# Kernel optimization log

Hardware: AMD Instinct MI355X
Metric: run time of the kernel (lower is better)

## Reference

```python
import jax, jax.numpy as jnp
import numpy as np

NUM_K_HEADS = 16
NUM_V_HEADS = 32
HEAD_K = 64
HEAD_V = 64
KERNEL = 4
KEY_DIM = NUM_K_HEADS * HEAD_K      # 1024
VAL_DIM = NUM_V_HEADS * HEAD_V      # 2048
CONV_DIM = 2 * KEY_DIM + VAL_DIM    # 4096
T = 2048


def setup_inputs() -> dict:
    key = jax.random.key(0)
    ks = jax.random.split(key, 6)
    return {
        "mixed_qkv": jax.random.normal(ks[0], (T, CONV_DIM), jnp.float32),
        "conv_state_in": jnp.zeros((1, KERNEL - 1, CONV_DIM), jnp.float32),
        "recurrent_state_in": jnp.zeros((1, NUM_V_HEADS, HEAD_K, HEAD_V), jnp.float32),
        "b": jax.random.normal(ks[1], (T, NUM_V_HEADS), jnp.float32),
        "a": jax.random.normal(ks[2], (T, NUM_V_HEADS), jnp.float32),
        "conv1d_weight": jax.random.normal(ks[3], (CONV_DIM, KERNEL), jnp.float32) * 0.1,
        "A_log": jax.random.normal(ks[4], (NUM_V_HEADS,), jnp.float32) * 0.1,
        "dt_bias": jax.random.normal(ks[5], (NUM_V_HEADS,), jnp.float32) * 0.1,
    }


def _causal_conv1d_prefill(x, weight, init_state):
    """Depthwise causal conv1d with silu. x:[T,D], weight:[D,W], init_state:[W-1,D]."""
    W = weight.shape[1]
    t = x.shape[0]
    padded = jnp.concatenate([init_state, x], axis=0)  # [T+W-1, D]
    out = padded[0:t] * weight[:, 0]
    for w in range(1, W):  # tiny fixed-width loop (W=4), fused by XLA
        out = out + padded[w:w + t] * weight[:, w]
    return jax.nn.silu(out)


def _l2norm(x, eps=1e-6):
    return x * jax.lax.rsqrt(jnp.sum(x * x, axis=-1, keepdims=True) + eps)


def reference(mixed_qkv, conv_state_in, recurrent_state_in, b, a, conv1d_weight, A_log, dt_bias):
    # --- causal conv over the prefill sequence (batch slice [:1] as in the module) ---
    conv_out = _causal_conv1d_prefill(mixed_qkv, conv1d_weight, conv_state_in[0])  # [T, CONV_DIM]
    t = conv_out.shape[0]

    # --- split into q/k/v heads ---
    q = conv_out[:, :KEY_DIM].reshape(t, NUM_K_HEADS, HEAD_K)
    k = conv_out[:, KEY_DIM:2 * KEY_DIM].reshape(t, NUM_K_HEADS, HEAD_K)
    v = conv_out[:, 2 * KEY_DIM:].reshape(t, NUM_V_HEADS, HEAD_V)
    rep = NUM_V_HEADS // NUM_K_HEADS
    if rep > 1:
        q = jnp.repeat(q, rep, axis=1)
        k = jnp.repeat(k, rep, axis=1)

    # --- gates ---
    beta = jax.nn.sigmoid(b.astype(jnp.float32))                       # [T, H]
    g = -jnp.exp(A_log)[None] * jax.nn.softplus(a.astype(jnp.float32) + dt_bias[None])  # [T, H]

    # --- qk l2-norm and scale (use_qk_l2norm=True) ---
    qn = _l2norm(q) * (HEAD_K ** -0.5)
    kn = _l2norm(k)

    # --- gated delta-rule recurrence over time ---
    def step(S, inp):
        q_t, k_t, v_t, g_t, b_t = inp  # [H,dk],[H,dk],[H,dv],[H],[H]
        S = S * jnp.exp(g_t)[:, None, None]                      # decay
        kv = jnp.einsum('hkv,hk->hv', S, k_t)                    # memory read
        u = b_t[:, None] * (v_t - kv)                            # delta update
        S = S + jnp.einsum('hk,hv->hkv', k_t, u)
        o = jnp.einsum('hkv,hk->hv', S, q_t)
        return S, o

    S0 = recurrent_state_in[0]  # [H, dk, dv]
    _, core_attn_out = jax.lax.scan(step, S0, (qn, kn, v, g, beta))
    return core_attn_out  # [T, H_v, head_v_dim]
```

## Files before the change

kernel.cpp:

```cpp
#include <hip/hip_runtime.h>
#include <math.h>

#define T_LEN   2048
#define NKH     16
#define NVH     32
#define HD      64
#define KEY_DIM 1024
#define VAL_DIM 2048
#define CONV_DIM 4096
#define NCHUNK  32
#define CL      64

typedef float fl4 __attribute__((ext_vector_type(4)));

__device__ __forceinline__ float sigmoid_f(float x) { return 1.f / (1.f + __expf(-x)); }
__device__ __forceinline__ float rdlane(float v, int i) {
    return __int_as_float(__builtin_amdgcn_readlane(__float_as_int(v), i));
}

__global__ __launch_bounds__(256) void prep_kernel(
    const float* __restrict__ x,
    const float* __restrict__ cs,
    const float* __restrict__ w,
    const float* __restrict__ bsrc,
    const float* __restrict__ a,
    const float* __restrict__ A_log,
    const float* __restrict__ dt_bias,
    float* __restrict__ qn,
    float* __restrict__ kn,
    float* __restrict__ vb,
    float* __restrict__ g,
    float* __restrict__ beta)
{
    const int t   = blockIdx.x;
    const int tid = threadIdx.x;
    const int d0  = tid * 16;

    fl4 r4[4];
    #pragma unroll
    for (int grp = 0; grp < 4; ++grp) {
        const int d = d0 + grp * 4;
        fl4 xv[4], wq[4];
        #pragma unroll
        for (int wi = 0; wi < 4; ++wi) {
            const int row = t - 3 + wi;
            const float* src = (row >= 0) ? (x + (size_t)row * CONV_DIM + d)
                                          : (cs + (size_t)(row + 3) * CONV_DIM + d);
            xv[wi] = *(const fl4*)src;
        }
        #pragma unroll
        for (int j = 0; j < 4; ++j) wq[j] = *(const fl4*)(w + (size_t)(d + j) * 4);
        #pragma unroll
        for (int j = 0; j < 4; ++j) {
            float acc = xv[0][j] * wq[j][0];
            acc = fmaf(xv[1][j], wq[j][1], acc);
            acc = fmaf(xv[2][j], wq[j][2], acc);
            acc = fmaf(xv[3][j], wq[j][3], acc);
            r4[grp][j] = acc * sigmoid_f(acc);
        }
    }

    if (tid < 128) {
        float ss = 0.f;
        #pragma unroll
        for (int grp = 0; grp < 4; ++grp)
            #pragma unroll
            for (int j = 0; j < 4; ++j) ss = fmaf(r4[grp][j], r4[grp][j], ss);
        ss += __shfl_xor(ss, 1);
        ss += __shfl_xor(ss, 2);
        const bool is_q = (tid < 64);
        float scale = (is_q ? 0.125f : 1.0f) / sqrtf(ss + 1e-6f);
        float* dst = is_q ? (qn + (size_t)t * KEY_DIM + d0)
                          : (kn + (size_t)t * KEY_DIM + (d0 - KEY_DIM));
        #pragma unroll
        for (int grp = 0; grp < 4; ++grp) {
            fl4 o;
            #pragma unroll
            for (int j = 0; j < 4; ++j) o[j] = r4[grp][j] * scale;
            *(fl4*)(dst + grp * 4) = o;
        }
    } else {
        const int hh = (d0 - 2 * KEY_DIM) >> 6;
        const float bb = sigmoid_f(bsrc[(size_t)t * NVH + hh]);
        float* dst = vb + (size_t)t * VAL_DIM + (d0 - 2 * KEY_DIM);
        #pragma unroll
        for (int grp = 0; grp < 4; ++grp) {
            fl4 o;
            #pragma unroll
            for (int j = 0; j < 4; ++j) o[j] = r4[grp][j] * bb;
            *(fl4*)(dst + grp * 4) = o;
        }
    }

    if (tid < 32) {
        float av = a[(size_t)t * NVH + tid] + dt_bias[tid];
        float sp = fmaxf(av, 0.f) + log1pf(__expf(-fabsf(av)));
        g[(size_t)t * NVH + tid]    = -__expf(A_log[tid]) * sp;
        beta[(size_t)t * NVH + tid] = sigmoid_f(bsrc[(size_t)t * NVH + tid]);
    }
}

__global__ __launch_bounds__(256) void phase1_kernel(
    const float* __restrict__ qn, const float* __restrict__ kn,
    const float* __restrict__ gws, const float* __restrict__ bws,
    float* __restrict__ gam_g, float* __restrict__ bg_g,
    float* __restrict__ KT_g, float* __restrict__ QT_g,
    float* __restrict__ MTt_g, float* __restrict__ SUt_g)
{
    const int bid = blockIdx.x;
    const int c = bid >> 5, h = bid & 31, kh = h >> 1;
    const int tid = threadIdx.x, lane = tid & 63, wv = tid >> 6;

    __shared__ float Ks[64][68], Qs[64][68], Am[64][68], Tm[64][68];
    __shared__ float Gs[64], Dend[64], Bet[64];
    __shared__ float Xs[4][16][17];

    #pragma unroll
    for (int p = 0; p < 4; ++p) {
        int idx = p * 256 + tid;
        int t = idx >> 4, i4 = (idx & 15) * 4;
        *(fl4*)&Ks[t][i4] = *(const fl4*)&kn[(size_t)(c*64+t)*KEY_DIM + kh*64 + i4];
        *(fl4*)&Qs[t][i4] = *(const fl4*)&qn[(size_t)(c*64+t)*KEY_DIM + kh*64 + i4];
    }
    for (int idx = tid; idx < 64*64; idx += 256) {
        int t = idx >> 6, s = idx & 63;
        Tm[t][s] = (t == s) ? 1.f : 0.f;
    }
    if (tid < 64) {
        float gv = gws[(size_t)(c*64+lane)*NVH + h];
        #pragma unroll
        for (int d = 1; d < 64; d <<= 1) {
            float nv = __shfl_up(gv, d);
            if (lane >= d) gv += nv;
        }
        Gs[lane] = gv;
        float g63 = __shfl(gv, 63);
        Dend[lane] = __expf(g63 - gv);
        float bb = bws[(size_t)(c*64+lane)*NVH + h];
        Bet[lane] = bb;
        float ga = __expf(gv);
        gam_g[(size_t)(c*NVH+h)*64 + lane] = ga;
        bg_g[(size_t)(c*NVH+h)*64 + lane]  = ga * bb;
    }
    __syncthreads();

    if ((h & 1) == 0) {
        float* kdst = KT_g + (size_t)(c*NKH + kh)*64*64;
        float* qdst = QT_g + (size_t)(c*NKH + kh)*64*64;
        const int t = lane;
        #pragma unroll
        for (int ii = 0; ii < 16; ++ii) {
            int i = wv*16 + ii;
            kdst[i*64 + t] = Ks[t][i];
            qdst[i*64 + t] = Qs[t][i];
        }
    }

    float accK[16], accQ[16];
    {
        #pragma unroll
        for (int j = 0; j < 16; ++j) { accK[j] = 0.f; accQ[j] = 0.f; }
        const int t = lane, sbase = wv * 16;
        for (int i4 = 0; i4 < 64; i4 += 4) {
            fl4 kt = *(const fl4*)&Ks[t][i4];
            fl4 qt = *(const fl4*)&Qs[t][i4];
            #pragma unroll
            for (int sj = 0; sj < 16; ++sj) {
                fl4 ks = *(const fl4*)&Ks[sbase + sj][i4];
                accK[sj] += kt[0]*ks[0] + kt[1]*ks[1] + kt[2]*ks[2] + kt[3]*ks[3];
                accQ[sj] += qt[0]*ks[0] + qt[1]*ks[1] + qt[2]*ks[2] + qt[3]*ks[3];
            }
        }
    }
    __syncthreads();
    {
        const int t = lane, sbase = wv * 16;
        const float gt = Gs[t], bt = Bet[t];
        #pragma unroll
        for (int sj = 0; sj < 16; ++sj) {
            int s = sbase + sj;
            float e = __expf(gt - Gs[s]);
            Am[t][s] = (s < t)  ? bt * e * accK[sj] : 0.f;
            Qs[t][s] = (s <= t) ? e * accQ[sj] : 0.f;
        }
    }
    __syncthreads();

    {
        const int base = wv * 16;
        const int s = lane & 15;
        float Tc[16];
        #pragma unroll
        for (int j = 0; j < 16; ++j) Tc[j] = (j == s) ? 1.f : 0.f;
        #pragma unroll
        for (int t = 1; t < 16; ++t) {
            float acc = 0.f;
            #pragma unroll
            for (int il = 0; il < 16; ++il) {
                if (il < t) acc = fmaf(Am[base + t][base + il], Tc[il], acc);
            }
            Tc[t] = (s < t) ? -acc : Tc[t];
        }
        if (lane < 16) {
            #pragma unroll
            for (int j = 0; j < 16; ++j)
                Tm[base + j][base + s] = Tc[j];
        }
    }
    for (int L = 1; L <= 3; ++L) {
        __syncthreads();
        if (wv < 4 - L) {
            const int J = wv, I = wv + L;
            const int r = lane & 15, cg = lane >> 4;
            float X[4] = {0.f,0.f,0.f,0.f};
            for (int Kb = J; Kb < I; ++Kb) {
                #pragma unroll
                for (int p = 0; p < 16; ++p) {
                    float av = Am[I*16 + r][Kb*16 + p];
                    #pragma unroll
                    for (int mm = 0; mm < 4; ++mm)
                        X[mm] += av * Tm[Kb*16 + p][J*16 + cg + 4*mm];
                }
            }
            #pragma unroll
            for (int mm = 0; mm < 4; ++mm) Xs[wv][r][cg + 4*mm] = X[mm];
            float Y[4] = {0.f,0.f,0.f,0.f};
            #pragma unroll
            for (int p = 0; p < 16; ++p) {
                float td = Tm[I*16 + r][I*16 + p];
                #pragma unroll
                for (int mm = 0; mm < 4; ++mm)
                    Y[mm] += td * Xs[wv][p][cg + 4*mm];
            }
            #pragma unroll
            for (int mm = 0; mm < 4; ++mm)
                Tm[I*16 + r][J*16 + cg + 4*mm] = -Y[mm];
        }
    }
    __syncthreads();

    {
        float acc[16];
        #pragma unroll
        for (int j = 0; j < 16; ++j) acc[j] = 0.f;
        const int t = lane, sbase = wv * 16;
        for (int i = 0; i < 64; i += 4) {
            fl4 mv4 = *(const fl4*)&Qs[t][i];
            #pragma unroll
            for (int r = 0; r < 4; ++r) {
                fl4 ta = *(const fl4*)&Tm[i+r][sbase + 0];
                fl4 tb = *(const fl4*)&Tm[i+r][sbase + 4];
                fl4 tc = *(const fl4*)&Tm[i+r][sbase + 8];
                fl4 td = *(const fl4*)&Tm[i+r][sbase + 12];
                #pragma unroll
                for (int q = 0; q < 4; ++q) {
                    acc[q]      = fmaf(mv4[r], ta[q], acc[q]);
                    acc[4 + q]  = fmaf(mv4[r], tb[q], acc[4 + q]);
                    acc[8 + q]  = fmaf(mv4[r], tc[q], acc[8 + q]);
                    acc[12 + q] = fmaf(mv4[r], td[q], acc[12 + q]);
                }
            }
        }
        float* dst = MTt_g + (size_t)(c*NVH + h)*64*64;
        #pragma unroll
        for (int sj = 0; sj < 16; ++sj)
            dst[(sbase + sj)*64 + t] = acc[sj];
    }
    {
        float acc[16];
        #pragma unroll
        for (int j = 0; j < 16; ++j) acc[j] = 0.f;
        const int d = lane, sbase = wv * 16;
        for (int t = 0; t < 64; ++t) {
            float kd = Ks[t][d] * Dend[t];
            fl4 ta = *(const fl4*)&Tm[t][sbase + 0];
            fl4 tb = *(const fl4*)&Tm[t][sbase + 4];
            fl4 tc = *(const fl4*)&Tm[t][sbase + 8];
            fl4 td = *(const fl4*)&Tm[t][sbase + 12];
            #pragma unroll
            for (int q = 0; q < 4; ++q) {
                acc[q]      = fmaf(kd, ta[q], acc[q]);
                acc[4 + q]  = fmaf(kd, tb[q], acc[4 + q]);
                acc[8 + q]  = fmaf(kd, tc[q], acc[8 + q]);
                acc[12 + q] = fmaf(kd, td[q], acc[12 + q]);
            }
        }
        float* dst = SUt_g + (size_t)(c*NVH + h)*64*64;
        #pragma unroll
        for (int sj = 0; sj < 16; ++sj)
            dst[(sbase + sj)*64 + d] = acc[sj];
    }
}

__global__ __launch_bounds__(512) void phase2_kernel(
    const float* __restrict__ vbp, const float* __restrict__ gam_g,
    const float* __restrict__ bg_g, const float* __restrict__ KT_g,
    const float* __restrict__ QT_g, const float* __restrict__ MTt_g,
    const float* __restrict__ SUt_g, const float* __restrict__ rs0,
    float* __restrict__ out)
{
    const int bid = blockIdx.x;
    const int h = bid & 31, jg = bid >> 5, kh = h >> 1;
    const int tid = threadIdx.x, lane = tid & 63, wv = tid >> 6;
    const int mv = wv >> 2;
    const int jb = (wv & 3) * 2;

    __shared__ float bufA[8192];
    __shared__ float bufB[8192];
    __shared__ float s0s[64][9], wshs[64][9], o1s[64][9];

    {
        int d = tid >> 3, j = tid & 7;
        s0s[d][j] = rs0[((size_t)h*64 + d)*64 + jg*8 + j];
    }

    const int base = tid * 4;

    fl4 rA0, rA1, rA2, rA3;
    {
        const float* kt = KT_g + (size_t)kh * 4096 + base;
        const float* qt = QT_g + (size_t)kh * 4096 + base;
        rA0 = *(const fl4*)(kt); rA1 = *(const fl4*)(kt + 2048);
        rA2 = *(const fl4*)(qt); rA3 = *(const fl4*)(qt + 2048);
    }

    for (int c = 0; c < NCHUNK; ++c) {
        *(fl4*)&bufA[base       ] = rA0; *(fl4*)&bufA[base + 2048] = rA1;
        *(fl4*)&bufA[base + 4096] = rA2; *(fl4*)&bufA[base + 6144] = rA3;

        fl4 rB0, rB1, rB2, rB3;
        {
            const float* mt = MTt_g + (size_t)(c*NVH + h)*4096 + base;
            const float* su = SUt_g + (size_t)(c*NVH + h)*4096 + base;
            rB0 = *(const fl4*)(mt); rB1 = *(const fl4*)(mt + 2048);
            rB2 = *(const fl4*)(su); rB3 = *(const fl4*)(su + 2048);
        }

        const float* gamc = gam_g + (size_t)(c*NVH + h)*64;
        const float* bgc  = bg_g  + (size_t)(c*NVH + h)*64;
        const float gend = gamc[63];
        float vb0 = 0.f, vb1 = 0.f, bgl = 0.f, gml = 0.f;
        if (mv == 0) {
            const float* vp = &vbp[(size_t)(c*64 + lane)*VAL_DIM + h*64 + jg*8 + jb];
            vb0 = vp[0]; vb1 = vp[1];
            bgl = bgc[lane];
        } else {
            gml = gamc[lane];
        }

        __syncthreads();

        float sa0 = s0s[lane][jb], sa1 = s0s[lane][jb + 1];
        float a0 = 0.f, a1 = 0.f;
        {
            const float* mb = &bufA[mv * 4096 + lane];
            #pragma unroll
            for (int i = 0; i < 64; ++i) {
                float m = mb[i * 64];
                a0 = fmaf(m, rdlane(sa0, i), a0);
                a1 = fmaf(m, rdlane(sa1, i), a1);
            }
        }
        if (mv == 0) {
            wshs[lane][jb]     = vb0 - bgl * a0;
            wshs[lane][jb + 1] = vb1 - bgl * a1;
        } else {
            o1s[lane][jb]     = gml * a0;
            o1s[lane][jb + 1] = gml * a1;
        }
        __syncthreads();

        *(fl4*)&bufB[base       ] = rB0; *(fl4*)&bufB[base + 2048] = rB1;
        *(fl4*)&bufB[base + 4096] = rB2; *(fl4*)&bufB[base + 6144] = rB3;

        if (c + 1 < NCHUNK) {
            const float* kt = KT_g + (size_t)((c+1)*NKH + kh)*4096 + base;
            const float* qt = QT_g + (size_t)((c+1)*NKH + kh)*4096 + base;
            rA0 = *(const fl4*)(kt); rA1 = *(const fl4*)(kt + 2048);
            rA2 = *(const fl4*)(qt); rA3 = *(const fl4*)(qt + 2048);
        }
        __syncthreads();

        float sb0 = wshs[lane][jb], sb1 = wshs[lane][jb + 1];
        float b0 = 0.f, b1 = 0.f;
        {
            const float* mb = &bufB[mv * 4096 + lane];
            #pragma unroll
            for (int i = 0; i < 64; ++i) {
                float m = mb[i * 64];
                b0 = fmaf(m, rdlane(sb0, i), b0);
                b1 = fmaf(m, rdlane(sb1, i), b1);
            }
        }
        if (mv == 0) {
            float* op = &out[(size_t)(c*64 + lane)*VAL_DIM + h*64 + jg*8 + jb];
            op[0] = o1s[lane][jb]     + b0;
            op[1] = o1s[lane][jb + 1] + b1;
        } else {
            s0s[lane][jb]     = gend * s0s[lane][jb]     + b0;
            s0s[lane][jb + 1] = gend * s0s[lane][jb + 1] + b1;
        }
        __syncthreads();
    }
}

#define LOADSTEP(KA, QA, VV, GG, BB, tt) {                                     \
    _Pragma("unroll")                                                          \
    for (int i = 0; i < 4; ++i) {                                              \
        KA[i] = *(const fl4*)(kp + (size_t)(tt) * KEY_DIM + i * 4);            \
        QA[i] = *(const fl4*)(qp + (size_t)(tt) * KEY_DIM + i * 4);            \
    }                                                                          \
    VV = vp[(size_t)(tt) * VAL_DIM];                                           \
    GG = gp[(size_t)(tt) * NVH];                                               \
    BB = bp[(size_t)(tt) * NVH];                                               \
}

#define COMPUTE(KA, QA, VV, GG, BB, tt) {                                      \
    const float dec = __expf(GG);                                              \
    float c0 = 0.f, c1 = 0.f, c2 = 0.f, c3 = 0.f;                              \
    _Pragma("unroll")                                                          \
    for (int i = 0; i < 4; ++i) {                                              \
        S[i*4+0] *= dec; S[i*4+1] *= dec; S[i*4+2] *= dec; S[i*4+3] *= dec;    \
        c0 = fmaf(S[i*4+0], KA[i][0], c0);                                     \
        c1 = fmaf(S[i*4+1], KA[i][1], c1);                                     \
        c2 = fmaf(S[i*4+2], KA[i][2], c2);                                     \
        c3 = fmaf(S[i*4+3], KA[i][3], c3);                                     \
    }                                                                          \
    float kv = (c0 + c1) + (c2 + c3);                                          \
    kv += __shfl_xor(kv, 1);                                                   \
    kv += __shfl_xor(kv, 2);                                                   \
    const float u = VV - BB * kv;                                              \
    float o0 = 0.f, o1 = 0.f, o2 = 0.f, o3 = 0.f;                              \
    _Pragma("unroll")                                                          \
    for (int i = 0; i < 4; ++i) {                                              \
        S[i*4+0] = fmaf(KA[i][0], u, S[i*4+0]);                                \
        S[i*4+1] = fmaf(KA[i][1], u, S[i*4+1]);                                \
        S[i*4+2] = fmaf(KA[i][2], u, S[i*4+2]);                                \
        S[i*4+3] = fmaf(KA[i][3], u, S[i*4+3]);                                \
        o0 = fmaf(S[i*4+0], QA[i][0], o0);                                     \
        o1 = fmaf(S[i*4+1], QA[i][1], o1);                                     \
        o2 = fmaf(S[i*4+2], QA[i][2], o2);                                     \
        o3 = fmaf(S[i*4+3], QA[i][3], o3);                                     \
    }                                                                          \
    float oo = (o0 + o1) + (o2 + o3);                                          \
    oo += __shfl_xor(oo, 1);                                                   \
    oo += __shfl_xor(oo, 2);                                                   \
    if (kg == 0) op[(size_t)(tt) * VAL_DIM] = oo;                              \
}

__global__ __launch_bounds__(256) void scan_kernel(
    const float* __restrict__ qn, const float* __restrict__ kn,
    const float* __restrict__ v, const float* __restrict__ g,
    const float* __restrict__ bet, const float* __restrict__ rs0,
    float* __restrict__ out)
{
    const int h    = blockIdx.x;
    const int kh   = h >> 1;
    const int tid  = threadIdx.x;
    const int vcol = tid >> 2;
    const int kg   = tid & 3;

    float S[16];
    #pragma unroll
    for (int j = 0; j < 16; ++j)
        S[j] = rs0[((size_t)h * HD + (kg * 16 + j)) * HD + vcol];

    const float* kp = kn + (size_t)kh * HD + kg * 16;
    const float* qp = qn + (size_t)kh * HD + kg * 16;
    const float* vp = v + (size_t)h * HD + vcol;
    const float* gp = g + h;
    const float* bp = bet + h;
    float*       op = out + (size_t)h * HD + vcol;

    fl4 ka0[4], qa0[4]; float vv0, gg0, bb0;
    fl4 ka1[4], qa1[4]; float vv1, gg1, bb1;

    LOADSTEP(ka0, qa0, vv0, gg0, bb0, 0);
    for (int t = 0; t < T_LEN; t += 2) {
        LOADSTEP(ka1, qa1, vv1, gg1, bb1, t + 1);
        COMPUTE(ka0, qa0, vv0, gg0, bb0, t);
        const int t2 = (t + 2 < T_LEN) ? (t + 2) : (T_LEN - 1);
        LOADSTEP(ka0, qa0, vv0, gg0, bb0, t2);
        COMPUTE(ka1, qa1, vv1, gg1, bb1, t + 1);
    }
}

extern "C" void kernel_launch(void* const* d_in, const int* in_sizes, int n_in,
                              void* d_out, int out_size, void* d_ws, size_t ws_size,
                              hipStream_t stream)
{
    const float* x       = (const float*)d_in[0];
    const float* cs      = (const float*)d_in[1];
    const float* rs0     = (const float*)d_in[2];
    const float* b       = (const float*)d_in[3];
    const float* a       = (const float*)d_in[4];
    const float* w       = (const float*)d_in[5];
    const float* A_log   = (const float*)d_in[6];
    const float* dt_bias = (const float*)d_in[7];
    float* out = (float*)d_out;

    float* ws = (float*)d_ws;
    size_t off = 0;
    float* qn  = ws + off; off += (size_t)T_LEN * KEY_DIM;
    float* kn  = ws + off; off += (size_t)T_LEN * KEY_DIM;
    float* vb  = ws + off; off += (size_t)T_LEN * VAL_DIM;
    float* g   = ws + off; off += (size_t)T_LEN * NVH;
    float* be  = ws + off; off += (size_t)T_LEN * NVH;
    float* gam = ws + off; off += (size_t)NCHUNK * NVH * 64;
    float* bg  = ws + off; off += (size_t)NCHUNK * NVH * 64;
    float* KT  = ws + off; off += (size_t)NCHUNK * NKH * 64 * 64;
    float* QT  = ws + off; off += (size_t)NCHUNK * NKH * 64 * 64;
    float* MTt = ws + off; off += (size_t)NCHUNK * NVH * 64 * 64;
    float* SUt = ws + off; off += (size_t)NCHUNK * NVH * 64 * 64;
    const size_t need = off * sizeof(float);

    prep_kernel<<<T_LEN, 256, 0, stream>>>(x, cs, w, b, a, A_log, dt_bias,
                                           qn, kn, vb, g, be);
    if (ws_size >= need) {
        phase1_kernel<<<NCHUNK * NVH, 256, 0, stream>>>(qn, kn, g, be,
                                                        gam, bg, KT, QT, MTt, SUt);
        phase2_kernel<<<NVH * 8, 512, 0, stream>>>(vb, gam, bg, KT, QT, MTt, SUt,
                                                   rs0, out);
    } else {
        scan_kernel<<<NVH, 256, 0, stream>>>(qn, kn, vb, g, be, rs0, out);
    }
}
```

Baseline: 283.9 us.

## Share K/Q Gram work across head pairs and prefetch phase2 operands one chunk ahead

phase1 now runs one block per (chunk, key head) and processes both value heads that share that key head. The K/Q loads, the KK^T/QK^T Gram products and the KT/QT transposes are done once and reused for both heads, which halves the block count and removes duplicated work. phase2 prefetches MTt/SUt for the next chunk into registers, removes one __syncthreads per chunk, and splits each dot-product FMA chain into even/odd accumulators to add instruction-level parallelism. In exchange there are fewer blocks in phase1 (less parallelism), more registers live in phase2, and the summation order changes slightly.

```diff
diff --git a/kernel.cpp b/kernel.cpp
--- a/kernel.cpp
+++ b/kernel.cpp
@@ -108,11 +108,11 @@
     float* __restrict__ MTt_g, float* __restrict__ SUt_g)
 {
     const int bid = blockIdx.x;
-    const int c = bid >> 5, h = bid & 31, kh = h >> 1;
+    const int c = bid >> 4, kh = bid & 15;
     const int tid = threadIdx.x, lane = tid & 63, wv = tid >> 6;
 
     __shared__ float Ks[64][68], Qs[64][68], Am[64][68], Tm[64][68];
-    __shared__ float Gs[64], Dend[64], Bet[64];
+    __shared__ float Gs[2][64], Dend[2][64], Bet[2][64];
     __shared__ float Xs[4][16][17];
 
     #pragma unroll
@@ -126,25 +126,27 @@
         int t = idx >> 6, s = idx & 63;
         Tm[t][s] = (t == s) ? 1.f : 0.f;
     }
-    if (tid < 64) {
+    if (tid < 128) {
+        const int hh = wv;
+        const int h = 2*kh + hh;
         float gv = gws[(size_t)(c*64+lane)*NVH + h];
         #pragma unroll
         for (int d = 1; d < 64; d <<= 1) {
             float nv = __shfl_up(gv, d);
             if (lane >= d) gv += nv;
         }
-        Gs[lane] = gv;
+        Gs[hh][lane] = gv;
         float g63 = __shfl(gv, 63);
-        Dend[lane] = __expf(g63 - gv);
+        Dend[hh][lane] = __expf(g63 - gv);
         float bb = bws[(size_t)(c*64+lane)*NVH + h];
-        Bet[lane] = bb;
+        Bet[hh][lane] = bb;
         float ga = __expf(gv);
         gam_g[(size_t)(c*NVH+h)*64 + lane] = ga;
         bg_g[(size_t)(c*NVH+h)*64 + lane]  = ga * bb;
     }
     __syncthreads();
 
-    if ((h & 1) == 0) {
+    {
         float* kdst = KT_g + (size_t)(c*NKH + kh)*64*64;
         float* qdst = QT_g + (size_t)(c*NKH + kh)*64*64;
         const int t = lane;
@@ -172,123 +174,128 @@
             }
         }
     }
-    __syncthreads();
-    {
-        const int t = lane, sbase = wv * 16;
-        const float gt = Gs[t], bt = Bet[t];
-        #pragma unroll
-        for (int sj = 0; sj < 16; ++sj) {
-            int s = sbase + sj;
-            float e = __expf(gt - Gs[s]);
-            Am[t][s] = (s < t)  ? bt * e * accK[sj] : 0.f;
-            Qs[t][s] = (s <= t) ? e * accQ[sj] : 0.f;
-        }
-    }
-    __syncthreads();
-
-    {
-        const int base = wv * 16;
-        const int s = lane & 15;
-        float Tc[16];
-        #pragma unroll
-        for (int j = 0; j < 16; ++j) Tc[j] = (j == s) ? 1.f : 0.f;
-        #pragma unroll
-        for (int t = 1; t < 16; ++t) {
-            float acc = 0.f;
-            #pragma unroll
-            for (int il = 0; il < 16; ++il) {
-                if (il < t) acc = fmaf(Am[base + t][base + il], Tc[il], acc);
-            }
-            Tc[t] = (s < t) ? -acc : Tc[t];
-        }
-        if (lane < 16) {
-            #pragma unroll
-            for (int j = 0; j < 16; ++j)
-                Tm[base + j][base + s] = Tc[j];
-        }
-    }
-    for (int L = 1; L <= 3; ++L) {
+
+    #pragma unroll
+    for (int hh = 0; hh < 2; ++hh) {
+        const int h = 2*kh + hh;
         __syncthreads();
-        if (wv < 4 - L) {
-            const int J = wv, I = wv + L;
-            const int r = lane & 15, cg = lane >> 4;
-            float X[4] = {0.f,0.f,0.f,0.f};
-            for (int Kb = J; Kb < I; ++Kb) {
+        {
+            const int t = lane, sbase = wv * 16;
+            const float gt = Gs[hh][t], bt = Bet[hh][t];
+            #pragma unroll
+            for (int sj = 0; sj < 16; ++sj) {
+                int s = sbase + sj;
+                float e = __expf(gt - Gs[hh][s]);
+                Am[t][s] = (s < t)  ? bt * e * accK[sj] : 0.f;
+                Qs[t][s] = (s <= t) ? e * accQ[sj] : 0.f;
+            }
+        }
+        __syncthreads();
+
+        {
+            const int base = wv * 16;
+            const int s = lane & 15;
+            float Tc[16];
+            #pragma unroll
+            for (int j = 0; j < 16; ++j) Tc[j] = (j == s) ? 1.f : 0.f;
+            #pragma unroll
+            for (int t = 1; t < 16; ++t) {
+                float acc = 0.f;
+                #pragma unroll
+                for (int il = 0; il < 16; ++il) {
+                    if (il < t) acc = fmaf(Am[base + t][base + il], Tc[il], acc);
+                }
+                Tc[t] = (s < t) ? -acc : Tc[t];
+            }
+            if (lane < 16) {
+                #pragma unroll
+                for (int j = 0; j < 16; ++j)
+                    Tm[base + j][base + s] = Tc[j];
+            }
+        }
+        for (int L = 1; L <= 3; ++L) {
+            __syncthreads();
+            if (wv < 4 - L) {
+                const int J = wv, I = wv + L;
+                const int r = lane & 15, cg = lane >> 4;
+                float X[4] = {0.f,0.f,0.f,0.f};
+                for (int Kb = J; Kb < I; ++Kb) {
+                    #pragma unroll
+                    for (int p = 0; p < 16; ++p) {
+                        float av = Am[I*16 + r][Kb*16 + p];
+                        #pragma unroll
+                        for (int mm = 0; mm < 4; ++mm)
+                            X[mm] += av * Tm[Kb*16 + p][J*16 + cg + 4*mm];
+                    }
+                }
+                #pragma unroll
+                for (int mm = 0; mm < 4; ++mm) Xs[wv][r][cg + 4*mm] = X[mm];
+                float Y[4] = {0.f,0.f,0.f,0.f};
                 #pragma unroll
                 for (int p = 0; p < 16; ++p) {
-                    float av = Am[I*16 + r][Kb*16 + p];
+                    float td = Tm[I*16 + r][I*16 + p];
                     #pragma unroll
                     for (int mm = 0; mm < 4; ++mm)
-                        X[mm] += av * Tm[Kb*16 + p][J*16 + cg + 4*mm];
+                        Y[mm] += td * Xs[wv][p][cg + 4*mm];
                 }
-            }
-            #pragma unroll
-            for (int mm = 0; mm < 4; ++mm) Xs[wv][r][cg + 4*mm] = X[mm];
-            float Y[4] = {0.f,0.f,0.f,0.f};
-            #pragma unroll
-            for (int p = 0; p < 16; ++p) {
-                float td = Tm[I*16 + r][I*16 + p];
                 #pragma unroll
                 for (int mm = 0; mm < 4; ++mm)
-                    Y[mm] += td * Xs[wv][p][cg + 4*mm];
-            }
-            #pragma unroll
-            for (int mm = 0; mm < 4; ++mm)
-                Tm[I*16 + r][J*16 + cg + 4*mm] = -Y[mm];
-        }
-    }
-    __syncthreads();
-
-    {
-        float acc[16];
-        #pragma unroll
-        for (int j = 0; j < 16; ++j) acc[j] = 0.f;
-        const int t = lane, sbase = wv * 16;
-        for (int i = 0; i < 64; i += 4) {
-            fl4 mv4 = *(const fl4*)&Qs[t][i];
-            #pragma unroll
-            for (int r = 0; r < 4; ++r) {
-                fl4 ta = *(const fl4*)&Tm[i+r][sbase + 0];
-                fl4 tb = *(const fl4*)&Tm[i+r][sbase + 4];
-                fl4 tc = *(const fl4*)&Tm[i+r][sbase + 8];
-                fl4 td = *(const fl4*)&Tm[i+r][sbase + 12];
+                    Tm[I*16 + r][J*16 + cg + 4*mm] = -Y[mm];
+            }
+        }
+        __syncthreads();
+
+        {
+            float acc[16];
+            #pragma unroll
+            for (int j = 0; j < 16; ++j) acc[j] = 0.f;
+            const int t = lane, sbase = wv * 16;
+            for (int i = 0; i < 64; i += 4) {
+                fl4 mv4 = *(const fl4*)&Qs[t][i];
+                #pragma unroll
+                for (int r = 0; r < 4; ++r) {
+                    fl4 ta = *(const fl4*)&Tm[i+r][sbase + 0];
+                    fl4 tb = *(const fl4*)&Tm[i+r][sbase + 4];
+                    fl4 tc = *(const fl4*)&Tm[i+r][sbase + 8];
+                    fl4 td = *(const fl4*)&Tm[i+r][sbase + 12];
+                    #pragma unroll
+                    for (int q = 0; q < 4; ++q) {
+                        acc[q]      = fmaf(mv4[r], ta[q], acc[q]);
+                        acc[4 + q]  = fmaf(mv4[r], tb[q], acc[4 + q]);
+                        acc[8 + q]  = fmaf(mv4[r], tc[q], acc[8 + q]);
+                        acc[12 + q] = fmaf(mv4[r], td[q], acc[12 + q]);
+                    }
+                }
+            }
+            float* dst = MTt_g + (size_t)(c*NVH + h)*64*64;
+            #pragma unroll
+            for (int sj = 0; sj < 16; ++sj)
+                dst[(sbase + sj)*64 + t] = acc[sj];
+        }
+        {
+            float acc[16];
+            #pragma unroll
+            for (int j = 0; j < 16; ++j) acc[j] = 0.f;
+            const int d = lane, sbase = wv * 16;
+            for (int t = 0; t < 64; ++t) {
+                float kd = Ks[t][d] * Dend[hh][t];
+                fl4 ta = *(const fl4*)&Tm[t][sbase + 0];
+                fl4 tb = *(const fl4*)&Tm[t][sbase + 4];
+                fl4 tc = *(const fl4*)&Tm[t][sbase + 8];
+                fl4 td = *(const fl4*)&Tm[t][sbase + 12];
                 #pragma unroll
                 for (int q = 0; q < 4; ++q) {
-                    acc[q]      = fmaf(mv4[r], ta[q], acc[q]);
-                    acc[4 + q]  = fmaf(mv4[r], tb[q], acc[4 + q]);
-                    acc[8 + q]  = fmaf(mv4[r], tc[q], acc[8 + q]);
-                    acc[12 + q] = fmaf(mv4[r], td[q], acc[12 + q]);
+                    acc[q]      = fmaf(kd, ta[q], acc[q]);
+                    acc[4 + q]  = fmaf(kd, tb[q], acc[4 + q]);
+                    acc[8 + q]  = fmaf(kd, tc[q], acc[8 + q]);
+                    acc[12 + q] = fmaf(kd, td[q], acc[12 + q]);
                 }
             }
-        }
-        float* dst = MTt_g + (size_t)(c*NVH + h)*64*64;
-        #pragma unroll
-        for (int sj = 0; sj < 16; ++sj)
-            dst[(sbase + sj)*64 + t] = acc[sj];
-    }
-    {
-        float acc[16];
-        #pragma unroll
-        for (int j = 0; j < 16; ++j) acc[j] = 0.f;
-        const int d = lane, sbase = wv * 16;
-        for (int t = 0; t < 64; ++t) {
-            float kd = Ks[t][d] * Dend[t];
-            fl4 ta = *(const fl4*)&Tm[t][sbase + 0];
-            fl4 tb = *(const fl4*)&Tm[t][sbase + 4];
-            fl4 tc = *(const fl4*)&Tm[t][sbase + 8];
-            fl4 td = *(const fl4*)&Tm[t][sbase + 12];
-            #pragma unroll
-            for (int q = 0; q < 4; ++q) {
-                acc[q]      = fmaf(kd, ta[q], acc[q]);
-                acc[4 + q]  = fmaf(kd, tb[q], acc[4 + q]);
-                acc[8 + q]  = fmaf(kd, tc[q], acc[8 + q]);
-                acc[12 + q] = fmaf(kd, td[q], acc[12 + q]);
-            }
-        }
-        float* dst = SUt_g + (size_t)(c*NVH + h)*64*64;
-        #pragma unroll
-        for (int sj = 0; sj < 16; ++sj)
-            dst[(sbase + sj)*64 + d] = acc[sj];
+            float* dst = SUt_g + (size_t)(c*NVH + h)*64*64;
+            #pragma unroll
+            for (int sj = 0; sj < 16; ++sj)
+                dst[(sbase + sj)*64 + d] = acc[sj];
+        }
     }
 }
 
@@ -316,24 +323,26 @@
 
     const int base = tid * 4;
 
-    fl4 rA0, rA1, rA2, rA3;
+    fl4 rA0, rA1, rA2, rA3, rB0, rB1, rB2, rB3;
     {
         const float* kt = KT_g + (size_t)kh * 4096 + base;
         const float* qt = QT_g + (size_t)kh * 4096 + base;
         rA0 = *(const fl4*)(kt); rA1 = *(const fl4*)(kt + 2048);
         rA2 = *(const fl4*)(qt); rA3 = *(const fl4*)(qt + 2048);
+        const float* mt = MTt_g + (size_t)h * 4096 + base;
+        const float* su = SUt_g + (size_t)h * 4096 + base;
+        rB0 = *(const fl4*)(mt); rB1 = *(const fl4*)(mt + 2048);
+        rB2 = *(const fl4*)(su); rB3 = *(const fl4*)(su + 2048);
     }
 
     for (int c = 0; c < NCHUNK; ++c) {
         *(fl4*)&bufA[base       ] = rA0; *(fl4*)&bufA[base + 2048] = rA1;
         *(fl4*)&bufA[base + 4096] = rA2; *(fl4*)&bufA[base + 6144] = rA3;
-
-        fl4 rB0, rB1, rB2, rB3;
-        {
-            const float* mt = MTt_g + (size_t)(c*NVH + h)*4096 + base;
-            const float* su = SUt_g + (size_t)(c*NVH + h)*4096 + base;
-            rB0 = *(const fl4*)(mt); rB1 = *(const fl4*)(mt + 2048);
-            rB2 = *(const fl4*)(su); rB3 = *(const fl4*)(su + 2048);
+        if (c + 1 < NCHUNK) {
+            const float* kt = KT_g + (size_t)((c+1)*NKH + kh)*4096 + base;
+            const float* qt = QT_g + (size_t)((c+1)*NKH + kh)*4096 + base;
+            rA0 = *(const fl4*)(kt); rA1 = *(const fl4*)(kt + 2048);
+            rA2 = *(const fl4*)(qt); rA3 = *(const fl4*)(qt + 2048);
         }
 
         const float* gamc = gam_g + (size_t)(c*NVH + h)*64;
@@ -351,54 +360,62 @@
         __syncthreads();
 
         float sa0 = s0s[lane][jb], sa1 = s0s[lane][jb + 1];
-        float a0 = 0.f, a1 = 0.f;
+        float a0e = 0.f, a0o = 0.f, a1e = 0.f, a1o = 0.f;
         {
             const float* mb = &bufA[mv * 4096 + lane];
             #pragma unroll
-            for (int i = 0; i < 64; ++i) {
-                float m = mb[i * 64];
-                a0 = fmaf(m, rdlane(sa0, i), a0);
-                a1 = fmaf(m, rdlane(sa1, i), a1);
-            }
-        }
-        if (mv == 0) {
-            wshs[lane][jb]     = vb0 - bgl * a0;
-            wshs[lane][jb + 1] = vb1 - bgl * a1;
-        } else {
-            o1s[lane][jb]     = gml * a0;
-            o1s[lane][jb + 1] = gml * a1;
-        }
-        __syncthreads();
+            for (int i = 0; i < 64; i += 2) {
+                float m0 = mb[i * 64], m1 = mb[(i + 1) * 64];
+                a0e = fmaf(m0, rdlane(sa0, i), a0e);
+                a1e = fmaf(m0, rdlane(sa1, i), a1e);
+                a0o = fmaf(m1, rdlane(sa0, i + 1), a0o);
+                a1o = fmaf(m1, rdlane(sa1, i + 1), a1o);
+            }
+        }
+        {
+            float a0 = a0e + a0o, a1 = a1e + a1o;
+            if (mv == 0) {
+                wshs[lane][jb]     = vb0 - bgl * a0;
+                wshs[lane][jb + 1] = vb1 - bgl * a1;
+            } else {
+                o1s[lane][jb]     = gml * a0;
+                o1s[lane][jb + 1] = gml * a1;
+            }
+        }
 
         *(fl4*)&bufB[base       ] = rB0; *(fl4*)&bufB[base + 2048] = rB1;
         *(fl4*)&bufB[base + 4096] = rB2; *(fl4*)&bufB[base + 6144] = rB3;
-
         if (c + 1 < NCHUNK) {
-            const float* kt = KT_g + (size_t)((c+1)*NKH + kh)*4096 + base;
-            const float* qt = QT_g + (size_t)((c+1)*NKH + kh)*4096 + base;
-            rA0 = *(const fl4*)(kt); rA1 = *(const fl4*)(kt + 2048);
-            rA2 = *(const fl4*)(qt); rA3 = *(const fl4*)(qt + 2048);
+            const float* mt = MTt_g + (size_t)((c+1)*NVH + h)*4096 + base;
+            const float* su = SUt_g + (size_t)((c+1)*NVH + h)*4096 + base;
+            rB0 = *(const fl4*)(mt); rB1 = *(const fl4*)(mt + 2048);
+            rB2 = *(const fl4*)(su); rB3 = *(const fl4*)(su + 2048);
         }
         __syncthreads();
 
         float sb0 = wshs[lane][jb], sb1 = wshs[lane][jb + 1];
-        float b0 = 0.f, b1 = 0.f;
+        float b0e = 0.f, b0o = 0.f, b1e = 0.f, b1o = 0.f;
         {
             const float* mb = &bufB[mv * 4096 + lane];
             #pragma unroll
-            for (int i = 0; i < 64; ++i) {
-                float m = mb[i * 64];
-                b0 = fmaf(m, rdlane(sb0, i), b0);
-                b1 = fmaf(m, rdlane(sb1, i), b1);
-            }
-        }
-        if (mv == 0) {
-            float* op = &out[(size_t)(c*64 + lane)*VAL_DIM + h*64 + jg*8 + jb];
-            op[0] = o1s[lane][jb]     + b0;
-            op[1] = o1s[lane][jb + 1] + b1;
-        } else {
-            s0s[lane][jb]     = gend * s0s[lane][jb]     + b0;
-            s0s[lane][jb + 1] = gend * s0s[lane][jb + 1] + b1;
+            for (int i = 0; i < 64; i += 2) {
+                float m0 = mb[i * 64], m1 = mb[(i + 1) * 64];
+                b0e = fmaf(m0, rdlane(sb0, i), b0e);
+                b1e = fmaf(m0, rdlane(sb1, i), b1e);
+                b0o = fmaf(m1, rdlane(sb0, i + 1), b0o);
+                b1o = fmaf(m1, rdlane(sb1, i + 1), b1o);
+            }
+        }
+        {
+            float b0 = b0e + b0o, b1 = b1e + b1o;
+            if (mv == 0) {
+                float* op = &out[(size_t)(c*64 + lane)*VAL_DIM + h*64 + jg*8 + jb];
+                op[0] = o1s[lane][jb]     + b0;
+                op[1] = o1s[lane][jb + 1] + b1;
+            } else {
+                s0s[lane][jb]     = gend * s0s[lane][jb]     + b0;
+                s0s[lane][jb + 1] = gend * s0s[lane][jb + 1] + b1;
+            }
         }
         __syncthreads();
     }
@@ -517,7 +534,7 @@
     prep_kernel<<<T_LEN, 256, 0, stream>>>(x, cs, w, b, a, A_log, dt_bias,
                                            qn, kn, vb, g, be);
     if (ws_size >= need) {
-        phase1_kernel<<<NCHUNK * NVH, 256, 0, stream>>>(qn, kn, g, be,
+        phase1_kernel<<<NCHUNK * NKH, 256, 0, stream>>>(qn, kn, g, be,
                                                         gam, bg, KT, QT, MTt, SUt);
         phase2_kernel<<<NVH * 8, 512, 0, stream>>>(vb, gam, bg, KT, QT, MTt, SUt,
                                                    rs0, out);
```

Result: faster. 272.9 us (-3.9%).
